# Kernel optimization log

Measured on AMD Instinct MI355X. Metric: run time of the kernel, lower is better.

## Reference

```python
import jax, jax.numpy as jnp
import numpy as np

# Dims: B=16 graphs, T=354 timesteps (l_max), N=64 nodes, H=128 model dim, NS=32 complex SSM modes

def setup_inputs() -> dict:
    key = jax.random.key(0)
    ks = jax.random.split(key, 10)
    B, T, N, H, NS = 16, 354, 64, 128, 32
    x = jax.random.normal(ks[0], (B, T, N), jnp.float32)
    W_in = jax.random.normal(ks[1], (H, 1), jnp.float32) * 0.5
    b_in = jnp.zeros((H,), jnp.float32)
    # S4D params: timescales log-uniform in [1e-3, 1e-1], A = -1/2 + i*pi*n (S4D-Lin init)
    log_dt = (jnp.log(0.001) + jax.random.uniform(ks[2], (H,), jnp.float32) * (jnp.log(0.1) - jnp.log(0.001))).astype(jnp.float32)
    A_re = -0.5 * jnp.ones((H, NS), jnp.float32)
    A_im = jnp.broadcast_to(np.pi * jnp.arange(NS, dtype=jnp.float32), (H, NS)).astype(jnp.float32) + 0.0
    C_re = jax.random.normal(ks[3], (H, NS), jnp.float32) * (0.5 ** 0.5)
    C_im = jax.random.normal(ks[4], (H, NS), jnp.float32) * (0.5 ** 0.5)
    D = jax.random.normal(ks[5], (H,), jnp.float32)
    W_out = jax.random.normal(ks[6], (2 * H, H), jnp.float32) * (1.0 / np.sqrt(H))
    b_out = jnp.zeros((2 * H,), jnp.float32)
    W_cls = jax.random.normal(ks[7], (1, H), jnp.float32) * (1.0 / np.sqrt(H))
    b_cls = jnp.zeros((1,), jnp.float32)
    return {"x": x, "W_in": W_in, "b_in": b_in, "log_dt": log_dt, "A_re": A_re, "A_im": A_im,
            "C_re": C_re, "C_im": C_im, "D": D, "W_out": W_out, "b_out": b_out,
            "W_cls": W_cls, "b_cls": b_cls}


def reference(x, W_in, b_in, log_dt, A_re, A_im, C_re, C_im, D, W_out, b_out, W_cls, b_cls):
    B, T, N = x.shape
    H = W_in.shape[0]
    # (B,T,N) -> (B*N, T, 1) per-node scalar series
    u = x.transpose(0, 2, 1).reshape(B * N, T, 1)
    u = u * W_in[:, 0] + b_in            # input_proj: (BN, T, H)
    u = u.transpose(0, 2, 1)             # transposed layout: (BN, H, L)
    # ---- S4D kernel (ZOH discretization, conjugate-pair 2*Re trick) ----
    dt = jnp.exp(log_dt)                 # (H,)
    A = A_re + 1j * A_im                 # (H, NS) complex64
    dtA = A * dt[:, None]                # (H, NS)
    C = C_re + 1j * C_im
    C_disc = C * (jnp.exp(dtA) - 1.0) / A
    l = jnp.arange(T)
    vand = jnp.exp(dtA[:, :, None] * l)  # Vandermonde (H, NS, L)
    K = 2.0 * jnp.real(jnp.einsum('hn,hnl->hl', C_disc, vand))  # (H, L)
    # ---- FFT causal long convolution + skip ----
    n_fft = 2 * T
    yf = jnp.fft.rfft(u, n_fft) * jnp.fft.rfft(K, n_fft)
    y = jnp.fft.irfft(yf, n_fft)[..., :T] + D[:, None] * u   # (BN, H, L)
    y = jax.nn.gelu(y)
    # dropout: identity at inference
    # ---- position-wise output linear H -> 2H, then GLU over channels ----
    g = jnp.einsum('bhl,gh->bgl', y, W_out) + b_out[:, None]  # (BN, 2H, L)
    z = g[:, :H] * jax.nn.sigmoid(g[:, H:])                    # (BN, H, L)
    # ---- pooling + classifier ----
    node_feats = z.mean(axis=-1).reshape(B, N, H)
    graph_feats = node_feats.mean(axis=1)                      # (B, H)
    logits = graph_feats @ W_cls.T + b_cls                     # (B, 1)
    return logits
```

## Files before the change

kernel.cpp:

```cpp
#include <hip/hip_runtime.h>
#include <hip/hip_bf16.h>


#define B_  16
#define T_  354
#define N_  64
#define H_  128
#define NS_ 32
#define BN_ (B_*N_)
#define TP_ 384
#define KW_ 512
#define G_  4
#define NG_ ((T_ + G_ - 1) / G_)

typedef __attribute__((ext_vector_type(8))) short bf16x8;
typedef __attribute__((ext_vector_type(4))) float f32x4;

static __device__ __forceinline__ unsigned short f32_to_bf16(float f) {
    unsigned int u = __float_as_uint(f);
    unsigned int r = 0x7FFFu + ((u >> 16) & 1u);
    return (unsigned short)((u + r) >> 16);
}

static __device__ __forceinline__ void gload_lds4(const void* g, void* l) {
    __builtin_amdgcn_global_load_lds(
        (const __attribute__((address_space(1))) unsigned int*)g,
        (__attribute__((address_space(3))) unsigned int*)l, 4, 0, 0);
}

__global__ void k_prep(const float* __restrict__ x, const float* __restrict__ W_out,
                       unsigned short* __restrict__ xbf, unsigned short* __restrict__ Wbf) {
    int id = blockIdx.x * blockDim.x + threadIdx.x;
    if (id < T_ * BN_) {
        int t  = id >> 10;
        int bn = id & 1023;
        float v = x[(bn >> 6) * (T_ * N_) + t * N_ + (bn & 63)];
        xbf[bn * TP_ + t] = f32_to_bf16(v);
    } else {
        int i = id - T_ * BN_;
        if (i < 2 * H_ * H_) Wbf[i] = f32_to_bf16(W_out[i]);
    }
}

__global__ __launch_bounds__(512) void k_kern(
        const float* __restrict__ log_dt,
        const float* __restrict__ A_re, const float* __restrict__ A_im,
        const float* __restrict__ C_re, const float* __restrict__ C_im,
        const float* __restrict__ b_in, const float* __restrict__ D,
        unsigned short* __restrict__ Krev, float* __restrict__ koff) {
    const int h = blockIdx.x;
    const int l = threadIdx.x;

    float val = 0.0f;
    if (l < T_) {
        float dt = expf(log_dt[h]);
        float fl = (float)l;
#pragma unroll 4
        for (int m = 0; m < NS_; m++) {
            float are = A_re[h * NS_ + m], aim = A_im[h * NS_ + m];
            float dre = are * dt, dim = aim * dt;
            float er  = expf(dre);
            float c1, s1; __sincosf(dim, &s1, &c1);
            float e_re = er * c1, e_im = er * s1;
            float m_re = e_re - 1.0f, m_im = e_im;
            float inv  = 1.0f / (are * are + aim * aim);
            float q_re = (m_re * are + m_im * aim) * inv;
            float q_im = (m_im * are - m_re * aim) * inv;
            float c_r = C_re[h * NS_ + m], c_i = C_im[h * NS_ + m];
            float cdre = c_r * q_re - c_i * q_im;
            float cdim = c_r * q_im + c_i * q_re;
            float el = expf(dre * fl);
            float cl, sl; __sincosf(dim * fl, &sl, &cl);
            val += el * (cdre * cl - cdim * sl);
        }
        val *= 2.0f;
        if (l == 0) val += D[h];
    }

    __shared__ float sc[512];
    sc[l] = (l < T_) ? val : 0.0f;
    __syncthreads();
    for (int off = 1; off < 512; off <<= 1) {
        float add = (l >= off) ? sc[l - off] : 0.0f;
        __syncthreads();
        sc[l] += add;
        __syncthreads();
    }

    if (l < T_) {
        koff[l * H_ + h] = b_in[h] * sc[l];
        unsigned short bv = f32_to_bf16(val);
#pragma unroll
        for (int r = 0; r < 8; r++)
            Krev[((size_t)r * H_ + h) * KW_ + (T_ - 1 - l) + r] = bv;
    }
}

__global__ __launch_bounds__(256, 2) void k_fused(
        const unsigned short* __restrict__ xbf,
        const unsigned short* __restrict__ Krev,
        const float* __restrict__ koff,
        const float* __restrict__ W_in,
        const unsigned short* __restrict__ Wbf,
        const float* __restrict__ b_out,
        float* __restrict__ node_sum) {
    __shared__ unsigned short A_lds[128 * 136];
    __shared__ unsigned short B_lds[128 * 136];

    const int tid  = threadIdx.x;
    const int w    = tid >> 6;
    const int lane = tid & 63;
    const int quad = lane >> 4;
    const int l16  = lane & 15;
    const int bn0  = blockIdx.x * 128;
    const int tg0  = blockIdx.y * G_;
    const int wm   = (w & 1) * 64;
    const int wn   = (w >> 1) * 64;

    float win[4], bo1[4], bo2[4];
#pragma unroll
    for (int nt = 0; nt < 4; nt++) {
        int c = wn + nt * 16 + l16;
        win[nt] = W_in[c];
        bo1[nt] = b_out[c];
        bo2[nt] = b_out[128 + c];
    }

    f32x4 zacc[4][4];
#pragma unroll
    for (int mt = 0; mt < 4; mt++)
#pragma unroll
        for (int nt = 0; nt < 4; nt++) zacc[mt][nt] = (f32x4){0.f, 0.f, 0.f, 0.f};

    for (int g = 0; g < G_; g++) {
        const int t = tg0 + g;
        if (t >= T_) break;
        const int nkb = (t >> 7) + 1;

        f32x4 acc[4][4];
#pragma unroll
        for (int mt = 0; mt < 4; mt++)
#pragma unroll
            for (int nt = 0; nt < 4; nt++) acc[mt][nt] = (f32x4){0.f, 0.f, 0.f, 0.f};

        for (int kb = 0; kb < nkb; kb++) {
            const int tau0 = kb << 7;
            const int L    = 353 - t + tau0;
            const int cp   = (-L) & 7;
            __syncthreads();
#pragma unroll 8
            for (int i = 0; i < 32; i++) {
                int r = w * 32 + i;
                gload_lds4(xbf + (size_t)(bn0 + r) * TP_ + tau0 + lane * 2,
                           &A_lds[r * 136]);
            }
#pragma unroll 8
            for (int i = 0; i < 32; i++) {
                int h = w * 32 + i;
                gload_lds4(Krev + ((size_t)cp * H_ + h) * KW_ + (L + cp) + lane * 2,
                           &B_lds[h * 136]);
            }
            __syncthreads();

#pragma unroll
            for (int ks = 0; ks < 4; ks++) {
                bf16x8 af[4], bfr[4];
#pragma unroll
                for (int mt = 0; mt < 4; mt++)
                    af[mt] = *(const bf16x8*)&A_lds[(wm + mt * 16 + l16) * 136 + ks * 32 + quad * 8];
#pragma unroll
                for (int nt = 0; nt < 4; nt++)
                    bfr[nt] = *(const bf16x8*)&B_lds[(wn + nt * 16 + l16) * 136 + ks * 32 + quad * 8];
#pragma unroll
                for (int nt = 0; nt < 4; nt++)
#pragma unroll
                    for (int mt = 0; mt < 4; mt++)
                        acc[mt][nt] = __builtin_amdgcn_mfma_f32_16x16x32_bf16(
                            af[mt], bfr[nt], acc[mt][nt], 0, 0, 0);
            }
        }

        float ko[4];
#pragma unroll
        for (int nt = 0; nt < 4; nt++) ko[nt] = koff[t * H_ + wn + nt * 16 + l16];

        __syncthreads();
#pragma unroll
        for (int mt = 0; mt < 4; mt++)
#pragma unroll
            for (int nt = 0; nt < 4; nt++)
#pragma unroll
                for (int rr = 0; rr < 4; rr++) {
                    float v = fmaf(acc[mt][nt][rr], win[nt], ko[nt]);
                    float a  = 0.7978845608028654f * fmaf(0.044715f, v * v * v, v);
                    float e  = __expf(2.0f * a);
                    float th = 1.0f - 2.0f / (e + 1.0f);
                    float ge = 0.5f * v * (1.0f + th);
                    A_lds[(wm + mt * 16 + quad * 4 + rr) * 136 + wn + nt * 16 + l16]
                        = f32_to_bf16(ge);
                }

#pragma unroll 8
        for (int i = 0; i < 32; i++) {
            int r = w * 32 + i;
            gload_lds4(Wbf + (size_t)r * H_ + lane * 2, &B_lds[r * 136]);
        }
        __syncthreads();

        f32x4 acc1[4][4];
#pragma unroll
        for (int mt = 0; mt < 4; mt++)
#pragma unroll
            for (int nt = 0; nt < 4; nt++) acc1[mt][nt] = (f32x4){0.f, 0.f, 0.f, 0.f};
#pragma unroll
        for (int ks = 0; ks < 4; ks++) {
            bf16x8 af[4], bfr[4];
#pragma unroll
            for (int mt = 0; mt < 4; mt++)
                af[mt] = *(const bf16x8*)&A_lds[(wm + mt * 16 + l16) * 136 + ks * 32 + quad * 8];
#pragma unroll
            for (int nt = 0; nt < 4; nt++)
                bfr[nt] = *(const bf16x8*)&B_lds[(wn + nt * 16 + l16) * 136 + ks * 32 + quad * 8];
#pragma unroll
            for (int nt = 0; nt < 4; nt++)
#pragma unroll
                for (int mt = 0; mt < 4; mt++)
                    acc1[mt][nt] = __builtin_amdgcn_mfma_f32_16x16x32_bf16(
                        af[mt], bfr[nt], acc1[mt][nt], 0, 0, 0);
        }
        __syncthreads();

#pragma unroll 8
        for (int i = 0; i < 32; i++) {
            int r = w * 32 + i;
            gload_lds4(Wbf + (size_t)(128 + r) * H_ + lane * 2, &B_lds[r * 136]);
        }
        __syncthreads();

        f32x4 acc2[4][4];
#pragma unroll
        for (int mt = 0; mt < 4; mt++)
#pragma unroll
            for (int nt = 0; nt < 4; nt++) acc2[mt][nt] = (f32x4){0.f, 0.f, 0.f, 0.f};
#pragma unroll
        for (int ks = 0; ks < 4; ks++) {
            bf16x8 af[4], bfr[4];
#pragma unroll
            for (int mt = 0; mt < 4; mt++)
                af[mt] = *(const bf16x8*)&A_lds[(wm + mt * 16 + l16) * 136 + ks * 32 + quad * 8];
#pragma unroll
            for (int nt = 0; nt < 4; nt++)
                bfr[nt] = *(const bf16x8*)&B_lds[(wn + nt * 16 + l16) * 136 + ks * 32 + quad * 8];
#pragma unroll
            for (int nt = 0; nt < 4; nt++)
#pragma unroll
                for (int mt = 0; mt < 4; mt++)
                    acc2[mt][nt] = __builtin_amdgcn_mfma_f32_16x16x32_bf16(
                        af[mt], bfr[nt], acc2[mt][nt], 0, 0, 0);
        }

#pragma unroll
        for (int mt = 0; mt < 4; mt++)
#pragma unroll
            for (int nt = 0; nt < 4; nt++)
#pragma unroll
                for (int rr = 0; rr < 4; rr++) {
                    float a  = acc1[mt][nt][rr] + bo1[nt];
                    float bs = acc2[mt][nt][rr] + bo2[nt];
                    float sg = 1.0f / (1.0f + __expf(-bs));
                    zacc[mt][nt][rr] += a * sg;
                }
    }

#pragma unroll
    for (int mt = 0; mt < 4; mt++)
#pragma unroll
        for (int nt = 0; nt < 4; nt++)
#pragma unroll
            for (int rr = 0; rr < 4; rr++) {
                int bn = bn0 + wm + mt * 16 + quad * 4 + rr;
                int j  = wn + nt * 16 + l16;
                atomicAdd(&node_sum[bn * H_ + j], zacc[mt][nt][rr]);
            }
}

__global__ void k_cls(const float* __restrict__ node_sum,
                      const float* __restrict__ W_cls, const float* __restrict__ b_cls,
                      float* __restrict__ out) {
    const int b = blockIdx.x, tid = threadIdx.x;
    float s = 0.0f;
    for (int i = tid; i < N_ * H_; i += 256)
        s += node_sum[b * (N_ * H_) + i] * W_cls[i & (H_ - 1)];
    __shared__ float red[256];
    red[tid] = s;
    __syncthreads();
    for (int off = 128; off > 0; off >>= 1) {
        if (tid < off) red[tid] += red[tid + off];
        __syncthreads();
    }
    if (tid == 0) out[b] = red[0] * (1.0f / (354.0f * 64.0f)) + b_cls[0];
}

extern "C" void kernel_launch(void* const* d_in, const int* in_sizes, int n_in,
                              void* d_out, int out_size, void* d_ws, size_t ws_size,
                              hipStream_t stream) {
    const float* x      = (const float*)d_in[0];
    const float* W_in   = (const float*)d_in[1];
    const float* b_in   = (const float*)d_in[2];
    const float* log_dt = (const float*)d_in[3];
    const float* A_re   = (const float*)d_in[4];
    const float* A_im   = (const float*)d_in[5];
    const float* C_re   = (const float*)d_in[6];
    const float* C_im   = (const float*)d_in[7];
    const float* D      = (const float*)d_in[8];
    const float* W_out  = (const float*)d_in[9];
    const float* b_out  = (const float*)d_in[10];
    const float* W_cls  = (const float*)d_in[11];
    const float* b_cls  = (const float*)d_in[12];

    char* ws = (char*)d_ws;
    float*          node_sum = (float*)(ws + 0);
    unsigned short* xbf      = (unsigned short*)(ws + 524288);
    unsigned short* Krev     = (unsigned short*)(ws + 1310720);
    float*          koff     = (float*)(ws + 2359296);
    unsigned short* Wbf      = (unsigned short*)(ws + 2540544);

    hipMemsetAsync(ws, 0, 2359296, stream);
    k_prep<<<dim3((T_ * BN_ + 2 * H_ * H_ + 255) / 256), dim3(256), 0, stream>>>(
        x, W_out, xbf, Wbf);
    k_kern<<<dim3(H_), dim3(512), 0, stream>>>(
        log_dt, A_re, A_im, C_re, C_im, b_in, D, Krev, koff);
    k_fused<<<dim3(BN_ / 128, NG_), dim3(256), 0, stream>>>(
        xbf, Krev, koff, W_in, Wbf, b_out, node_sum);
    k_cls<<<dim3(B_), dim3(256), 0, stream>>>(node_sum, W_cls, b_cls, (float*)d_out);
}
```

Measured before the change: 255.1 us.

## Keep W_out in registers, halve node tile, transpose MFMA roles, merge prep kernels

The fused kernel now processes 64 nodes per block instead of 128. It computes the convolution with K as the A operand and x as the B operand, so the GELU output is written transposed into LDS and feeds the output GEMM directly. W_out fragments are loaded once per block into registers, which removes the two per-timestep LDS reloads of W_out and their barriers. The two preprocessing kernels are merged into one launch, and GELU uses a sigmoid form. This raises register pressure, and doubling the block count doubles the K-tile loads from global memory across the grid.

```diff
diff --git a/kernel.cpp b/kernel.cpp
--- a/kernel.cpp
+++ b/kernel.cpp
@@ -10,6 +10,7 @@
 #define BN_ (B_*N_)
 #define TP_ 384
 #define KW_ 512
+#define PAD_ 136
 #define G_  4
 #define NG_ ((T_ + G_ - 1) / G_)
 
@@ -28,26 +29,35 @@
         (__attribute__((address_space(3))) unsigned int*)l, 4, 0, 0);
 }
 
-__global__ void k_prep(const float* __restrict__ x, const float* __restrict__ W_out,
-                       unsigned short* __restrict__ xbf, unsigned short* __restrict__ Wbf) {
-    int id = blockIdx.x * blockDim.x + threadIdx.x;
-    if (id < T_ * BN_) {
-        int t  = id >> 10;
-        int bn = id & 1023;
-        float v = x[(bn >> 6) * (T_ * N_) + t * N_ + (bn & 63)];
-        xbf[bn * TP_ + t] = f32_to_bf16(v);
-    } else {
-        int i = id - T_ * BN_;
-        if (i < 2 * H_ * H_) Wbf[i] = f32_to_bf16(W_out[i]);
-    }
-}
-
-__global__ __launch_bounds__(512) void k_kern(
+static __device__ __forceinline__ float gelu_f(float v) {
+    float v2 = v * v;
+    float x  = v * fmaf(0.0713548162726f, v2, 1.5957691216057f);
+    float sg = 1.0f / (1.0f + __expf(-x));
+    return v * sg;
+}
+
+__global__ __launch_bounds__(512) void k_pre(
         const float* __restrict__ log_dt,
         const float* __restrict__ A_re, const float* __restrict__ A_im,
         const float* __restrict__ C_re, const float* __restrict__ C_im,
         const float* __restrict__ b_in, const float* __restrict__ D,
-        unsigned short* __restrict__ Krev, float* __restrict__ koff) {
+        const float* __restrict__ x, const float* __restrict__ W_out,
+        unsigned short* __restrict__ Krev, float* __restrict__ koff,
+        unsigned short* __restrict__ xbf, unsigned short* __restrict__ Wbf) {
+    if (blockIdx.x >= H_) {
+        int id = (blockIdx.x - H_) * 512 + threadIdx.x;
+        if (id < T_ * BN_) {
+            int t  = id >> 10;
+            int bn = id & 1023;
+            float v = x[(bn >> 6) * (T_ * N_) + t * N_ + (bn & 63)];
+            xbf[bn * TP_ + t] = f32_to_bf16(v);
+        } else {
+            int i = id - T_ * BN_;
+            if (i < 2 * H_ * H_) Wbf[i] = f32_to_bf16(W_out[i]);
+        }
+        return;
+    }
+
     const int h = blockIdx.x;
     const int l = threadIdx.x;
 
@@ -104,31 +114,40 @@
         const unsigned short* __restrict__ Wbf,
         const float* __restrict__ b_out,
         float* __restrict__ node_sum) {
-    __shared__ unsigned short A_lds[128 * 136];
-    __shared__ unsigned short B_lds[128 * 136];
+    __shared__ unsigned short x_lds[64 * PAD_];
+    __shared__ unsigned short k_lds[128 * PAD_];
 
     const int tid  = threadIdx.x;
     const int w    = tid >> 6;
     const int lane = tid & 63;
-    const int quad = lane >> 4;
+    const int q    = lane >> 4;
     const int l16  = lane & 15;
-    const int bn0  = blockIdx.x * 128;
+    const int bn0  = blockIdx.x * 64;
     const int tg0  = blockIdx.y * G_;
-    const int wm   = (w & 1) * 64;
-    const int wn   = (w >> 1) * 64;
-
-    float win[4], bo1[4], bo2[4];
-#pragma unroll
-    for (int nt = 0; nt < 4; nt++) {
-        int c = wn + nt * 16 + l16;
-        win[nt] = W_in[c];
-        bo1[nt] = b_out[c];
-        bo2[nt] = b_out[128 + c];
-    }
-
-    f32x4 zacc[4][4];
-#pragma unroll
-    for (int mt = 0; mt < 4; mt++)
+
+    bf16x8 wfrag[4][4];
+#pragma unroll
+    for (int mt = 0; mt < 4; mt++) {
+        int jb = 32 * w + 16 * (mt & 1) + 128 * (mt >> 1);
+#pragma unroll
+        for (int ks = 0; ks < 4; ks++)
+            wfrag[mt][ks] = *(const bf16x8*)(Wbf + (size_t)(jb + l16) * H_ + ks * 32 + q * 8);
+    }
+
+    float win[2][4], bo1[2][4], bo2[2][4];
+#pragma unroll
+    for (int mt = 0; mt < 2; mt++)
+#pragma unroll
+        for (int rr = 0; rr < 4; rr++) {
+            int hj = 32 * w + 16 * mt + 4 * q + rr;
+            win[mt][rr] = W_in[hj];
+            bo1[mt][rr] = b_out[hj];
+            bo2[mt][rr] = b_out[128 + hj];
+        }
+
+    f32x4 zacc[2][4];
+#pragma unroll
+    for (int mt = 0; mt < 2; mt++)
 #pragma unroll
         for (int nt = 0; nt < 4; nt++) zacc[mt][nt] = (f32x4){0.f, 0.f, 0.f, 0.f};
 
@@ -137,149 +156,112 @@
         if (t >= T_) break;
         const int nkb = (t >> 7) + 1;
 
-        f32x4 acc[4][4];
-#pragma unroll
-        for (int mt = 0; mt < 4; mt++)
-#pragma unroll
-            for (int nt = 0; nt < 4; nt++) acc[mt][nt] = (f32x4){0.f, 0.f, 0.f, 0.f};
+        float ko[2][4];
+#pragma unroll
+        for (int mt = 0; mt < 2; mt++)
+#pragma unroll
+            for (int rr = 0; rr < 4; rr++)
+                ko[mt][rr] = koff[t * H_ + 32 * w + 16 * mt + 4 * q + rr];
+
+        f32x4 cacc[2][4];
+#pragma unroll
+        for (int mt = 0; mt < 2; mt++)
+#pragma unroll
+            for (int nt = 0; nt < 4; nt++) cacc[mt][nt] = (f32x4){0.f, 0.f, 0.f, 0.f};
 
         for (int kb = 0; kb < nkb; kb++) {
             const int tau0 = kb << 7;
             const int L    = 353 - t + tau0;
             const int cp   = (-L) & 7;
             __syncthreads();
+#pragma unroll
+            for (int i = 0; i < 16; i++) {
+                int r = w * 16 + i;
+                gload_lds4(xbf + (size_t)(bn0 + r) * TP_ + tau0 + lane * 2,
+                           &x_lds[r * PAD_]);
+            }
 #pragma unroll 8
             for (int i = 0; i < 32; i++) {
-                int r = w * 32 + i;
-                gload_lds4(xbf + (size_t)(bn0 + r) * TP_ + tau0 + lane * 2,
-                           &A_lds[r * 136]);
-            }
-#pragma unroll 8
-            for (int i = 0; i < 32; i++) {
-                int h = w * 32 + i;
-                gload_lds4(Krev + ((size_t)cp * H_ + h) * KW_ + (L + cp) + lane * 2,
-                           &B_lds[h * 136]);
+                int hr = w * 32 + i;
+                gload_lds4(Krev + ((size_t)cp * H_ + hr) * KW_ + (L + cp) + lane * 2,
+                           &k_lds[hr * PAD_]);
             }
             __syncthreads();
 
 #pragma unroll
             for (int ks = 0; ks < 4; ks++) {
-                bf16x8 af[4], bfr[4];
-#pragma unroll
-                for (int mt = 0; mt < 4; mt++)
-                    af[mt] = *(const bf16x8*)&A_lds[(wm + mt * 16 + l16) * 136 + ks * 32 + quad * 8];
+                bf16x8 af[2], bf[4];
+#pragma unroll
+                for (int mt = 0; mt < 2; mt++)
+                    af[mt] = *(const bf16x8*)&k_lds[(32 * w + 16 * mt + l16) * PAD_ + ks * 32 + q * 8];
 #pragma unroll
                 for (int nt = 0; nt < 4; nt++)
-                    bfr[nt] = *(const bf16x8*)&B_lds[(wn + nt * 16 + l16) * 136 + ks * 32 + quad * 8];
+                    bf[nt] = *(const bf16x8*)&x_lds[(16 * nt + l16) * PAD_ + ks * 32 + q * 8];
+#pragma unroll
+                for (int mt = 0; mt < 2; mt++)
+#pragma unroll
+                    for (int nt = 0; nt < 4; nt++)
+                        cacc[mt][nt] = __builtin_amdgcn_mfma_f32_16x16x32_bf16(
+                            af[mt], bf[nt], cacc[mt][nt], 0, 0, 0);
+            }
+        }
+
+        __syncthreads();
+#pragma unroll
+        for (int mt = 0; mt < 2; mt++)
+#pragma unroll
+            for (int nt = 0; nt < 4; nt++) {
+                unsigned short pk[4];
+#pragma unroll
+                for (int rr = 0; rr < 4; rr++) {
+                    float v = fmaf(cacc[mt][nt][rr], win[mt][rr], ko[mt][rr]);
+                    pk[rr] = f32_to_bf16(gelu_f(v));
+                }
+                *(uint2*)&x_lds[(16 * nt + l16) * PAD_ + 32 * w + 16 * mt + 4 * q]
+                    = *(const uint2*)pk;
+            }
+        __syncthreads();
+
+        f32x4 gacc[4][4];
+#pragma unroll
+        for (int mt = 0; mt < 4; mt++)
+#pragma unroll
+            for (int nt = 0; nt < 4; nt++) gacc[mt][nt] = (f32x4){0.f, 0.f, 0.f, 0.f};
+#pragma unroll
+        for (int ks = 0; ks < 4; ks++) {
+            bf16x8 yf[4];
+#pragma unroll
+            for (int nt = 0; nt < 4; nt++)
+                yf[nt] = *(const bf16x8*)&x_lds[(16 * nt + l16) * PAD_ + ks * 32 + q * 8];
+#pragma unroll
+            for (int mt = 0; mt < 4; mt++)
 #pragma unroll
                 for (int nt = 0; nt < 4; nt++)
-#pragma unroll
-                    for (int mt = 0; mt < 4; mt++)
-                        acc[mt][nt] = __builtin_amdgcn_mfma_f32_16x16x32_bf16(
-                            af[mt], bfr[nt], acc[mt][nt], 0, 0, 0);
-            }
-        }
-
-        float ko[4];
-#pragma unroll
-        for (int nt = 0; nt < 4; nt++) ko[nt] = koff[t * H_ + wn + nt * 16 + l16];
-
-        __syncthreads();
-#pragma unroll
-        for (int mt = 0; mt < 4; mt++)
+                    gacc[mt][nt] = __builtin_amdgcn_mfma_f32_16x16x32_bf16(
+                        wfrag[mt][ks], yf[nt], gacc[mt][nt], 0, 0, 0);
+        }
+
+#pragma unroll
+        for (int mt = 0; mt < 2; mt++)
 #pragma unroll
             for (int nt = 0; nt < 4; nt++)
 #pragma unroll
                 for (int rr = 0; rr < 4; rr++) {
-                    float v = fmaf(acc[mt][nt][rr], win[nt], ko[nt]);
-                    float a  = 0.7978845608028654f * fmaf(0.044715f, v * v * v, v);
-                    float e  = __expf(2.0f * a);
-                    float th = 1.0f - 2.0f / (e + 1.0f);
-                    float ge = 0.5f * v * (1.0f + th);
-                    A_lds[(wm + mt * 16 + quad * 4 + rr) * 136 + wn + nt * 16 + l16]
-                        = f32_to_bf16(ge);
-                }
-
-#pragma unroll 8
-        for (int i = 0; i < 32; i++) {
-            int r = w * 32 + i;
-            gload_lds4(Wbf + (size_t)r * H_ + lane * 2, &B_lds[r * 136]);
-        }
-        __syncthreads();
-
-        f32x4 acc1[4][4];
-#pragma unroll
-        for (int mt = 0; mt < 4; mt++)
-#pragma unroll
-            for (int nt = 0; nt < 4; nt++) acc1[mt][nt] = (f32x4){0.f, 0.f, 0.f, 0.f};
-#pragma unroll
-        for (int ks = 0; ks < 4; ks++) {
-            bf16x8 af[4], bfr[4];
-#pragma unroll
-            for (int mt = 0; mt < 4; mt++)
-                af[mt] = *(const bf16x8*)&A_lds[(wm + mt * 16 + l16) * 136 + ks * 32 + quad * 8];
-#pragma unroll
-            for (int nt = 0; nt < 4; nt++)
-                bfr[nt] = *(const bf16x8*)&B_lds[(wn + nt * 16 + l16) * 136 + ks * 32 + quad * 8];
-#pragma unroll
-            for (int nt = 0; nt < 4; nt++)
-#pragma unroll
-                for (int mt = 0; mt < 4; mt++)
-                    acc1[mt][nt] = __builtin_amdgcn_mfma_f32_16x16x32_bf16(
-                        af[mt], bfr[nt], acc1[mt][nt], 0, 0, 0);
-        }
-        __syncthreads();
-
-#pragma unroll 8
-        for (int i = 0; i < 32; i++) {
-            int r = w * 32 + i;
-            gload_lds4(Wbf + (size_t)(128 + r) * H_ + lane * 2, &B_lds[r * 136]);
-        }
-        __syncthreads();
-
-        f32x4 acc2[4][4];
-#pragma unroll
-        for (int mt = 0; mt < 4; mt++)
-#pragma unroll
-            for (int nt = 0; nt < 4; nt++) acc2[mt][nt] = (f32x4){0.f, 0.f, 0.f, 0.f};
-#pragma unroll
-        for (int ks = 0; ks < 4; ks++) {
-            bf16x8 af[4], bfr[4];
-#pragma unroll
-            for (int mt = 0; mt < 4; mt++)
-                af[mt] = *(const bf16x8*)&A_lds[(wm + mt * 16 + l16) * 136 + ks * 32 + quad * 8];
-#pragma unroll
-            for (int nt = 0; nt < 4; nt++)
-                bfr[nt] = *(const bf16x8*)&B_lds[(wn + nt * 16 + l16) * 136 + ks * 32 + quad * 8];
-#pragma unroll
-            for (int nt = 0; nt < 4; nt++)
-#pragma unroll
-                for (int mt = 0; mt < 4; mt++)
-                    acc2[mt][nt] = __builtin_amdgcn_mfma_f32_16x16x32_bf16(
-                        af[mt], bfr[nt], acc2[mt][nt], 0, 0, 0);
-        }
-
-#pragma unroll
-        for (int mt = 0; mt < 4; mt++)
-#pragma unroll
-            for (int nt = 0; nt < 4; nt++)
-#pragma unroll
-                for (int rr = 0; rr < 4; rr++) {
-                    float a  = acc1[mt][nt][rr] + bo1[nt];
-                    float bs = acc2[mt][nt][rr] + bo2[nt];
+                    float a  = gacc[mt][nt][rr] + bo1[mt][rr];
+                    float bs = gacc[mt + 2][nt][rr] + bo2[mt][rr];
                     float sg = 1.0f / (1.0f + __expf(-bs));
                     zacc[mt][nt][rr] += a * sg;
                 }
     }
 
 #pragma unroll
-    for (int mt = 0; mt < 4; mt++)
+    for (int mt = 0; mt < 2; mt++)
 #pragma unroll
         for (int nt = 0; nt < 4; nt++)
 #pragma unroll
             for (int rr = 0; rr < 4; rr++) {
-                int bn = bn0 + wm + mt * 16 + quad * 4 + rr;
-                int j  = wn + nt * 16 + l16;
+                int bn = bn0 + 16 * nt + l16;
+                int j  = 32 * w + 16 * mt + 4 * q + rr;
                 atomicAdd(&node_sum[bn * H_ + j], zacc[mt][nt][rr]);
             }
 }
@@ -326,11 +308,10 @@
     unsigned short* Wbf      = (unsigned short*)(ws + 2540544);
 
     hipMemsetAsync(ws, 0, 2359296, stream);
-    k_prep<<<dim3((T_ * BN_ + 2 * H_ * H_ + 255) / 256), dim3(256), 0, stream>>>(
-        x, W_out, xbf, Wbf);
-    k_kern<<<dim3(H_), dim3(512), 0, stream>>>(
-        log_dt, A_re, A_im, C_re, C_im, b_in, D, Krev, koff);
-    k_fused<<<dim3(BN_ / 128, NG_), dim3(256), 0, stream>>>(
+    const int prep_blocks = (T_ * BN_ + 2 * H_ * H_ + 511) / 512;
+    k_pre<<<dim3(H_ + prep_blocks), dim3(512), 0, stream>>>(
+        log_dt, A_re, A_im, C_re, C_im, b_in, D, x, W_out, Krev, koff, xbf, Wbf);
+    k_fused<<<dim3(BN_ / 64, NG_), dim3(256), 0, stream>>>(
         xbf, Krev, koff, W_in, Wbf, b_out, node_sum);
     k_cls<<<dim3(B_), dim3(256), 0, stream>>>(node_sum, W_cls, b_cls, (float*)d_out);
 }
```

New measurement: 312.5 us. +22.5%, slower.
